# Kernel tuning notes

Hardware: AMD Instinct MI355X
Metric: run time of the kernel (lower is better)

The kernel has to match this reference:

```python
import jax, jax.numpy as jnp
import numpy as np

N, IN_DIM, OUT_DIM, H = 1024, 128, 128, 4
D = OUT_DIM // H  # head_dim = 32
NEG_SLOPE = 0.2
MASK_VAL = -1e9
LN_EPS = 1e-5


def setup_inputs() -> dict:
    key = jax.random.key(0)
    k = jax.random.split(key, 8)
    h = jax.random.normal(k[0], (N, IN_DIM), dtype=jnp.float32)
    adj = jax.random.randint(k[1], (N, N), 0, 2, dtype=jnp.int32)
    adj = adj.at[jnp.arange(N), jnp.arange(N)].set(1)  # self-loops
    s = 1.0 / np.sqrt(IN_DIM)
    W_l = jax.random.normal(k[2], (IN_DIM, OUT_DIM), dtype=jnp.float32) * s
    W_r = jax.random.normal(k[3], (IN_DIM, OUT_DIM), dtype=jnp.float32) * s
    W_v = jax.random.normal(k[4], (IN_DIM, OUT_DIM), dtype=jnp.float32) * s
    a = jax.random.normal(k[5], (D,), dtype=jnp.float32) * (1.0 / np.sqrt(D))
    ln_g = jnp.ones((OUT_DIM,), dtype=jnp.float32)
    ln_b = jnp.zeros((OUT_DIM,), dtype=jnp.float32)
    return {"h": h, "adj": adj, "W_l": W_l, "W_r": W_r, "W_v": W_v,
            "a": a, "ln_g": ln_g, "ln_b": ln_b}


def reference(h, adj, W_l, W_r, W_v, a, ln_g, ln_b):
    n = h.shape[0]
    Wlh = (h @ W_l).reshape(n, H, D)   # [N,H,D]
    Wrh = (h @ W_r).reshape(n, H, D)   # [N,H,D]
    # pairwise additive scores: pair[i,j,h,d] = Wlh[i] + Wrh[j]
    pair = Wlh[:, None, :, :] + Wrh[None, :, :, :]          # [N,N,H,D]
    pair = jnp.where(pair >= 0, pair, NEG_SLOPE * pair)      # leaky_relu(0.2)
    e = jnp.einsum('ijhd,d->ijh', pair, a)                   # [N,N,H]
    mask = (adj != 0)[:, :, None]                            # [N,N,1]
    e = jnp.where(mask, e, MASK_VAL)
    alpha = jax.nn.softmax(e, axis=1)                        # softmax over j
    v = (h @ W_v).reshape(n, H, D)                           # [N,H,D]
    agg = jnp.einsum('ijh,jhd->ihd', alpha, v).reshape(n, OUT_DIM)
    mu = jnp.mean(agg, axis=-1, keepdims=True)
    var = jnp.mean((agg - mu) ** 2, axis=-1, keepdims=True)
    y = (agg - mu) * jax.lax.rsqrt(var + LN_EPS) * ln_g + ln_b
    return jax.nn.relu(y)
```

## Files before the change

### kernel.cpp

```cpp
#include <hip/hip_runtime.h>
#include <cstdint>

typedef _Float16 f16;
typedef _Float16 f16x2 __attribute__((ext_vector_type(2)));
typedef _Float16 f16x4 __attribute__((ext_vector_type(4)));
typedef _Float16 f16x8 __attribute__((ext_vector_type(8)));
typedef float    f32x4 __attribute__((ext_vector_type(4)));
typedef unsigned short u16;
typedef unsigned int   u32;

#define LOG2E 1.44269504088896340736f

__device__ __forceinline__ f16x2 habs2(f16x2 v) {
    union { f16x2 h; u32 u; } x; x.h = v; x.u &= 0x7FFF7FFFu; return x.h;
}
#if __has_builtin(__builtin_amdgcn_fdot2)
__device__ __forceinline__ float fdot2f(f16x2 a, f16x2 b, float c) {
    return __builtin_amdgcn_fdot2(a, b, c, false);
}
#else
__device__ __forceinline__ float fdot2f(f16x2 a, f16x2 b, float c) {
    return c + (float)a.x * (float)b.x + (float)a.y * (float)b.y;
}
#endif
#if __has_builtin(__builtin_amdgcn_exp2f)
#define EXP2F __builtin_amdgcn_exp2f
#else
#define EXP2F exp2f
#endif

__global__ __launch_bounds__(384) void k1_proj(
        const float* __restrict__ Wl, const float* __restrict__ Wr,
        const float* __restrict__ Wv, const float* __restrict__ h,
        const float* __restrict__ a_,
        f16* __restrict__ Wlh, f16* __restrict__ WrL, f16* __restrict__ VL,
        float* __restrict__ AL, float* __restrict__ BR) {
    __shared__ __align__(16) f16 hS[4][128];
    const int t    = threadIdx.x;
    const int i0   = blockIdx.x * 4;
    const int wsel = t >> 7, col = t & 127;
    const int lane = t & 63;

    for (int e = t; e < 512; e += 384)
        ((f16*)hS)[e] = (f16)h[i0 * 128 + e];

    const float* W = (wsel == 0) ? Wl : ((wsel == 1) ? Wr : Wv);
    f16x2 w2[64];
    #pragma unroll
    for (int c2 = 0; c2 < 64; c2++) {
        f16x2 v;
        v.x = (f16)W[(2 * c2) * 128 + col];
        v.y = (f16)W[(2 * c2 + 1) * 128 + col];
        w2[c2] = v;
    }
    const float asc = 0.6f * a_[col & 31];
    __syncthreads();

    #pragma unroll
    for (int i = 0; i < 4; i++) {
        const int j = i0 + i;
        const f16x2* hr = (const f16x2*)hS[i];
        float acc = 0.f;
        #pragma unroll
        for (int c2 = 0; c2 < 64; c2++) acc = fdot2f(hr[c2], w2[c2], acc);
        const f16 hv = (f16)acc;
        const int hh = col >> 5, dd = col & 31;
        if (wsel == 0) {
            Wlh[j * 128 + col] = hv;
        } else if (wsel == 1) {
            WrL[((hh * 8 + (dd >> 2)) * 1024 + j) * 4 + (dd & 3)] = hv;
        } else {
            VL[(hh * 32 + dd) * 1024 + j] = hv;
        }
        if (wsel < 2) {
            float part = asc * acc;
            #pragma unroll
            for (int off = 1; off < 32; off <<= 1) part += __shfl_xor(part, off);
            if ((lane & 31) == 0) {
                if (wsel == 0) AL[j * 4 + hh] = part;
                else           BR[hh * 1024 + j] = part;
            }
        }
    }
}

__global__ __launch_bounds__(512) void GATv2Layer_84447646974220_kernel(
        const f16* __restrict__ Wlh, const f16* __restrict__ WrL,
        const f16* __restrict__ VL,  const int* __restrict__ adj,
        const float* __restrict__ AL, const float* __restrict__ BR,
        const float* __restrict__ a_, const float* __restrict__ ln_g,
        const float* __restrict__ ln_b, float* __restrict__ out) {

    __shared__ __align__(16) f16 ep[4][4][1024];
    __shared__ float aggS[2][4][128];
    __shared__ float redM[2][4][4];
    __shared__ float redS[2][4][4];

    const int t    = threadIdx.x;
    const int w    = t >> 6;
    const int lane = t & 63;
    const int hh   = w & 3;
    const int half = w >> 2;
    const int i0   = blockIdx.x * 4;

    f16x2 q2[16];
    #pragma unroll
    for (int d2 = 0; d2 < 16; d2++) {
        f16x2 q; q.x = (f16)(0.4f * a_[2 * d2]); q.y = (f16)(0.4f * a_[2 * d2 + 1]);
        q2[d2] = q;
    }
    f16x2 wl2[4][16];
    float al[4];
    #pragma unroll
    for (int ii = 0; ii < 4; ii++) {
        const f16x2* src = (const f16x2*)(Wlh + (i0 + ii) * 128 + hh * 32);
        #pragma unroll
        for (int c2 = 0; c2 < 16; c2++) wl2[ii][c2] = src[c2];
        al[ii] = AL[(i0 + ii) * 4 + hh];
    }

    float maxE[4];
    #pragma unroll
    for (int ii = 0; ii < 4; ii++) maxE[ii] = -__builtin_inff();

    #pragma unroll 1
    for (int jb = 0; jb < 8; jb++) {
        int j = half * 512 + jb * 64 + lane;
        f16x4 wr[8];
        #pragma unroll
        for (int c = 0; c < 8; c++)
            wr[c] = *(const f16x4*)(WrL + ((hh * 8 + c) * 1024 + j) * 4);
        int am[4];
        #pragma unroll
        for (int ii = 0; ii < 4; ii++) am[ii] = adj[(i0 + ii) * 1024 + j];
        float bj = BR[hh * 1024 + j];

        float e[4];
        #pragma unroll
        for (int ii = 0; ii < 4; ii++) e[ii] = al[ii];
        #pragma unroll
        for (int c = 0; c < 8; c++) {
            #pragma unroll
            for (int ii = 0; ii < 4; ii++) {
                f16x2 t0 = wl2[ii][2 * c]     + wr[c].lo;
                f16x2 t1 = wl2[ii][2 * c + 1] + wr[c].hi;
                e[ii] = fdot2f(q2[2 * c],     habs2(t0), e[ii]);
                e[ii] = fdot2f(q2[2 * c + 1], habs2(t1), e[ii]);
            }
        }
        #pragma unroll
        for (int ii = 0; ii < 4; ii++) {
            float v = am[ii] ? (e[ii] + bj) : -__builtin_inff();
            maxE[ii] = fmaxf(maxE[ii], v);
            ep[hh][ii][j] = (f16)v;
        }
    }

    #pragma unroll
    for (int ii = 0; ii < 4; ii++) {
        float M = maxE[ii];
        #pragma unroll
        for (int off = 32; off > 0; off >>= 1) M = fmaxf(M, __shfl_xor(M, off));
        if (lane == 0) redM[half][hh][ii] = M;
    }
    __syncthreads();

    #pragma unroll
    for (int ii = 0; ii < 4; ii++) {
        float M = fmaxf(redM[0][hh][ii], redM[1][hh][ii]);
        f16x8 v0 = *(f16x8*)&ep[hh][ii][half * 512 + lane * 8];
        float pb[8], l = 0.f;
        #pragma unroll
        for (int e = 0; e < 8; e++) pb[e] = EXP2F(((float)v0[e] - M) * LOG2E);
        #pragma unroll
        for (int e = 0; e < 8; e++) { v0[e] = (f16)pb[e]; l += pb[e]; }
        *(f16x8*)&ep[hh][ii][half * 512 + lane * 8] = v0;
        #pragma unroll
        for (int off = 32; off > 0; off >>= 1) l += __shfl_xor(l, off);
        if (lane == 0) redS[half][hh][ii] = l;
    }
    __syncthreads();

    float lr[4];
    #pragma unroll
    for (int ii = 0; ii < 4; ii++)
        lr[ii] = 1.0f / (redS[0][hh][ii] + redS[1][hh][ii]);

    f32x4 acc0 = {0.f, 0.f, 0.f, 0.f}, acc1 = {0.f, 0.f, 0.f, 0.f};
    const int q8  = (lane >> 4) << 3;
    const int m3  = lane & 3;
    const int n15 = lane & 15;

    #pragma unroll 1
    for (int jt4 = 0; jt4 < 4; jt4++) {
        int jt = half * 4 + jt4;
        #pragma unroll
        for (int kk = 0; kk < 4; kk++) {
            int ko = jt * 128 + kk * 32 + q8;
            f16x8 af = *(const f16x8*)&ep[hh][m3][ko];
            f16x8 b0 = *(const f16x8*)(VL + (hh * 32 + n15) * 1024 + ko);
            f16x8 b1 = *(const f16x8*)(VL + (hh * 32 + 16 + n15) * 1024 + ko);
            acc0 = __builtin_amdgcn_mfma_f32_16x16x32_f16(af, b0, acc0, 0, 0, 0);
            acc1 = __builtin_amdgcn_mfma_f32_16x16x32_f16(af, b1, acc1, 0, 0, 0);
        }
    }

    if (lane < 16) {
        #pragma unroll
        for (int r = 0; r < 4; r++) {
            aggS[half][r][hh * 32 + lane]      = acc0[r] * lr[r];
            aggS[half][r][hh * 32 + 16 + lane] = acc1[r] * lr[r];
        }
    }
    __syncthreads();

    if (w < 4) {
        float x0 = aggS[0][w][lane]      + aggS[1][w][lane];
        float x1 = aggS[0][w][lane + 64] + aggS[1][w][lane + 64];
        float s = x0 + x1, sq = x0 * x0 + x1 * x1;
        #pragma unroll
        for (int off = 32; off > 0; off >>= 1) {
            s  += __shfl_xor(s, off);
            sq += __shfl_xor(sq, off);
        }
        float mean = s * (1.f / 128.f);
        float var  = sq * (1.f / 128.f) - mean * mean;
        float rs   = rsqrtf(var + 1e-5f);
        float y0 = fmaxf((x0 - mean) * rs * ln_g[lane]      + ln_b[lane],      0.f);
        float y1 = fmaxf((x1 - mean) * rs * ln_g[lane + 64] + ln_b[lane + 64], 0.f);
        out[(i0 + w) * 128 + lane]      = y0;
        out[(i0 + w) * 128 + 64 + lane] = y1;
    }
}

extern "C" void kernel_launch(void* const* d_in, const int* in_sizes, int n_in,
                              void* d_out, int out_size, void* d_ws, size_t ws_size,
                              hipStream_t stream) {
    const float* h   = (const float*)d_in[0];
    const int*   adj = (const int*)d_in[1];
    const float* Wl  = (const float*)d_in[2];
    const float* Wr  = (const float*)d_in[3];
    const float* Wv  = (const float*)d_in[4];
    const float* a_  = (const float*)d_in[5];
    const float* g_  = (const float*)d_in[6];
    const float* b_  = (const float*)d_in[7];
    float* out = (float*)d_out;

    char* ws = (char*)d_ws;
    f16*   Wlh = (f16*)(ws);
    f16*   WrL = (f16*)(ws + 262144);
    f16*   VL  = (f16*)(ws + 524288);
    float* AL  = (float*)(ws + 786432);
    float* BR  = (float*)(ws + 802816);

    k1_proj<<<256, 384, 0, stream>>>(Wl, Wr, Wv, h, a_, Wlh, WrL, VL, AL, BR);
    GATv2Layer_84447646974220_kernel<<<256, 512, 0, stream>>>(
        Wlh, WrL, VL, adj, AL, BR, a_, g_, b_, out);
}
```

Baseline: 96.25 us.

## Fuse projection and attention kernels via cooperative grid sync, prefetch adjacency bitmasks

Merges the projection kernel into the attention kernel and joins the two phases with a cooperative grid-wide barrier, removing one kernel launch. Per-block Wl projections and the AL scores stay in shared memory, so they no longer round-trip through global memory. While the other warps compute projections, two spare warps pack the adjacency rows into 64-bit ballot masks in LDS, replacing repeated int32 adjacency loads in the main loop. The trade-off is the cost of the grid sync and fences, plus the requirement that all 256 blocks of 512 threads be co-resident.

```diff
diff --git a/kernel.cpp b/kernel.cpp
--- a/kernel.cpp
+++ b/kernel.cpp
@@ -1,5 +1,8 @@
 #include <hip/hip_runtime.h>
+#include <hip/hip_cooperative_groups.h>
 #include <cstdint>
+
+namespace cg = cooperative_groups;
 
 typedef _Float16 f16;
 typedef _Float16 f16x2 __attribute__((ext_vector_type(2)));
@@ -8,6 +11,7 @@
 typedef float    f32x4 __attribute__((ext_vector_type(4)));
 typedef unsigned short u16;
 typedef unsigned int   u32;
+typedef unsigned long long u64;
 
 #define LOG2E 1.44269504088896340736f
 
@@ -29,79 +33,94 @@
 #define EXP2F exp2f
 #endif
 
-__global__ __launch_bounds__(384) void k1_proj(
+__global__ __launch_bounds__(512) void GATv2Layer_84447646974220_kernel(
         const float* __restrict__ Wl, const float* __restrict__ Wr,
         const float* __restrict__ Wv, const float* __restrict__ h,
-        const float* __restrict__ a_,
-        f16* __restrict__ Wlh, f16* __restrict__ WrL, f16* __restrict__ VL,
-        float* __restrict__ AL, float* __restrict__ BR) {
-    __shared__ __align__(16) f16 hS[4][128];
-    const int t    = threadIdx.x;
-    const int i0   = blockIdx.x * 4;
-    const int wsel = t >> 7, col = t & 127;
-    const int lane = t & 63;
-
-    for (int e = t; e < 512; e += 384)
-        ((f16*)hS)[e] = (f16)h[i0 * 128 + e];
-
-    const float* W = (wsel == 0) ? Wl : ((wsel == 1) ? Wr : Wv);
-    f16x2 w2[64];
-    #pragma unroll
-    for (int c2 = 0; c2 < 64; c2++) {
-        f16x2 v;
-        v.x = (f16)W[(2 * c2) * 128 + col];
-        v.y = (f16)W[(2 * c2 + 1) * 128 + col];
-        w2[c2] = v;
-    }
-    const float asc = 0.6f * a_[col & 31];
-    __syncthreads();
-
-    #pragma unroll
-    for (int i = 0; i < 4; i++) {
-        const int j = i0 + i;
-        const f16x2* hr = (const f16x2*)hS[i];
-        float acc = 0.f;
-        #pragma unroll
-        for (int c2 = 0; c2 < 64; c2++) acc = fdot2f(hr[c2], w2[c2], acc);
-        const f16 hv = (f16)acc;
-        const int hh = col >> 5, dd = col & 31;
-        if (wsel == 0) {
-            Wlh[j * 128 + col] = hv;
-        } else if (wsel == 1) {
-            WrL[((hh * 8 + (dd >> 2)) * 1024 + j) * 4 + (dd & 3)] = hv;
-        } else {
-            VL[(hh * 32 + dd) * 1024 + j] = hv;
-        }
-        if (wsel < 2) {
-            float part = asc * acc;
-            #pragma unroll
-            for (int off = 1; off < 32; off <<= 1) part += __shfl_xor(part, off);
-            if ((lane & 31) == 0) {
-                if (wsel == 0) AL[j * 4 + hh] = part;
-                else           BR[hh * 1024 + j] = part;
-            }
-        }
-    }
-}
-
-__global__ __launch_bounds__(512) void GATv2Layer_84447646974220_kernel(
-        const f16* __restrict__ Wlh, const f16* __restrict__ WrL,
-        const f16* __restrict__ VL,  const int* __restrict__ adj,
-        const float* __restrict__ AL, const float* __restrict__ BR,
-        const float* __restrict__ a_, const float* __restrict__ ln_g,
-        const float* __restrict__ ln_b, float* __restrict__ out) {
+        const int* __restrict__ adj, const float* __restrict__ a_,
+        const float* __restrict__ ln_g, const float* __restrict__ ln_b,
+        f16* __restrict__ WrL, f16* __restrict__ VL, float* __restrict__ BR,
+        float* __restrict__ out) {
 
     __shared__ __align__(16) f16 ep[4][4][1024];
     __shared__ float aggS[2][4][128];
     __shared__ float redM[2][4][4];
     __shared__ float redS[2][4][4];
+    __shared__ __align__(16) f16 WlS[4][128];
+    __shared__ __align__(16) f16 hS[4][128];
+    __shared__ float ALs[4][4];
+    __shared__ u64 amaskS[4][16];
 
     const int t    = threadIdx.x;
+    const int lane = t & 63;
+    const int i0   = blockIdx.x * 4;
+
+    ((f16*)hS)[t] = (f16)h[i0 * 128 + t];
+
+    f16x2 w2[64];
+    float asc = 0.f;
+    const int wsel = t >> 7, col = t & 127;
+    if (t < 384) {
+        const float* W = (wsel == 0) ? Wl : ((wsel == 1) ? Wr : Wv);
+        #pragma unroll
+        for (int c2 = 0; c2 < 64; c2++) {
+            f16x2 v;
+            v.x = (f16)W[(2 * c2) * 128 + col];
+            v.y = (f16)W[(2 * c2 + 1) * 128 + col];
+            w2[c2] = v;
+        }
+        asc = 0.6f * a_[col & 31];
+    } else {
+        const int lw = t - 384;
+        const int wv = lw >> 6;
+        const int ln = lw & 63;
+        #pragma unroll
+        for (int r = 0; r < 2; r++) {
+            const int ii = wv * 2 + r;
+            #pragma unroll 1
+            for (int c = 0; c < 16; c++) {
+                int av = adj[(i0 + ii) * 1024 + c * 64 + ln];
+                u64 m = __ballot(av != 0);
+                if (ln == 0) amaskS[ii][c] = m;
+            }
+        }
+    }
+    __syncthreads();
+
+    if (t < 384) {
+        #pragma unroll
+        for (int i = 0; i < 4; i++) {
+            const int j = i0 + i;
+            const f16x2* hr = (const f16x2*)hS[i];
+            float acc = 0.f;
+            #pragma unroll
+            for (int c2 = 0; c2 < 64; c2++) acc = fdot2f(hr[c2], w2[c2], acc);
+            const f16 hv = (f16)acc;
+            const int hh = col >> 5, dd = col & 31;
+            if (wsel == 0) {
+                WlS[i][col] = hv;
+                float part = asc * acc;
+                #pragma unroll
+                for (int off = 1; off < 32; off <<= 1) part += __shfl_xor(part, off);
+                if ((t & 31) == 0) ALs[i][hh] = part;
+            } else if (wsel == 1) {
+                WrL[((hh * 8 + (dd >> 2)) * 1024 + j) * 4 + (dd & 3)] = hv;
+                float part = asc * acc;
+                #pragma unroll
+                for (int off = 1; off < 32; off <<= 1) part += __shfl_xor(part, off);
+                if ((t & 31) == 0) BR[hh * 1024 + j] = part;
+            } else {
+                VL[(hh * 32 + dd) * 1024 + j] = hv;
+            }
+        }
+    }
+
+    __threadfence();
+    cg::this_grid().sync();
+    __threadfence();
+
     const int w    = t >> 6;
-    const int lane = t & 63;
     const int hh   = w & 3;
     const int half = w >> 2;
-    const int i0   = blockIdx.x * 4;
 
     f16x2 q2[16];
     #pragma unroll
@@ -113,10 +132,10 @@
     float al[4];
     #pragma unroll
     for (int ii = 0; ii < 4; ii++) {
-        const f16x2* src = (const f16x2*)(Wlh + (i0 + ii) * 128 + hh * 32);
+        const f16x2* src = (const f16x2*)&WlS[ii][hh * 32];
         #pragma unroll
         for (int c2 = 0; c2 < 16; c2++) wl2[ii][c2] = src[c2];
-        al[ii] = AL[(i0 + ii) * 4 + hh];
+        al[ii] = ALs[ii][hh];
     }
 
     float maxE[4];
@@ -130,9 +149,9 @@
         #pragma unroll
         for (int c = 0; c < 8; c++)
             wr[c] = *(const f16x4*)(WrL + ((hh * 8 + c) * 1024 + j) * 4);
-        int am[4];
-        #pragma unroll
-        for (int ii = 0; ii < 4; ii++) am[ii] = adj[(i0 + ii) * 1024 + j];
+        u64 wm[4];
+        #pragma unroll
+        for (int ii = 0; ii < 4; ii++) wm[ii] = amaskS[ii][half * 8 + jb];
         float bj = BR[hh * 1024 + j];
 
         float e[4];
@@ -150,7 +169,8 @@
         }
         #pragma unroll
         for (int ii = 0; ii < 4; ii++) {
-            float v = am[ii] ? (e[ii] + bj) : -__builtin_inff();
+            bool ok = (wm[ii] >> lane) & 1ull;
+            float v = ok ? (e[ii] + bj) : -__builtin_inff();
             maxE[ii] = fmaxf(maxE[ii], v);
             ep[hh][ii][j] = (f16)v;
         }
@@ -247,13 +267,15 @@
     float* out = (float*)d_out;
 
     char* ws = (char*)d_ws;
-    f16*   Wlh = (f16*)(ws);
-    f16*   WrL = (f16*)(ws + 262144);
-    f16*   VL  = (f16*)(ws + 524288);
-    float* AL  = (float*)(ws + 786432);
-    float* BR  = (float*)(ws + 802816);
-
-    k1_proj<<<256, 384, 0, stream>>>(Wl, Wr, Wv, h, a_, Wlh, WrL, VL, AL, BR);
-    GATv2Layer_84447646974220_kernel<<<256, 512, 0, stream>>>(
-        Wlh, WrL, VL, adj, AL, BR, a_, g_, b_, out);
-}
+    f16*   WrL = (f16*)(ws);
+    f16*   VL  = (f16*)(ws + 262144);
+    float* BR  = (float*)(ws + 524288);
+
+    void* args[] = {
+        (void*)&Wl, (void*)&Wr, (void*)&Wv, (void*)&h, (void*)&adj,
+        (void*)&a_, (void*)&g_, (void*)&b_, (void*)&WrL, (void*)&VL,
+        (void*)&BR, (void*)&out
+    };
+    hipLaunchCooperativeKernel((const void*)GATv2Layer_84447646974220_kernel,
+                               dim3(256), dim3(512), args, 0, stream);
+}
```

Result: slower. 225.4 us (+134.1%).
